# Kernel tuning notes

Hardware: AMD Instinct MI355X
Metric: run time of the kernel (lower is better)

The kernel has to match this reference:

```python
import jax, jax.numpy as jnp
import numpy as np

N, E, D, H, C = 40000, 640000, 128, 4, 32  # nodes, edges, in_hid, heads, out_channels/head
NUM_NODE_TYPE, NUM_EDGE_TYPE = 8, 8
NEG_SLOPE = 0.2
EDGE_TYPE_SELF = 0


def setup_inputs() -> dict:
    key = jax.random.key(0)
    ks = jax.random.split(key, 12)
    x = jax.random.normal(ks[0], (N, D), dtype=jnp.float32)
    # build edges with no self-loops (the module filters src==dst before adding self-loops)
    src = jax.random.randint(ks[1], (E,), 0, N, dtype=jnp.int32)
    off = jax.random.randint(ks[2], (E,), 1, N, dtype=jnp.int32)
    dst = (src + off) % N
    edge_index = jnp.stack([src, dst])  # [2, E]
    node_type = jax.random.randint(ks[3], (N,), 0, NUM_NODE_TYPE, dtype=jnp.int32)
    edge_type = jax.random.randint(ks[4], (E,), 0, NUM_EDGE_TYPE, dtype=jnp.int32)
    g = 0.05
    Wq = jax.random.normal(ks[5], (H * C, D), dtype=jnp.float32) * g
    Wk = jax.random.normal(ks[6], (H * C, D), dtype=jnp.float32) * g
    Wv = jax.random.normal(ks[7], (H * C, D), dtype=jnp.float32) * g
    att_i = jax.random.normal(ks[8], (1, H, C), dtype=jnp.float32) * g
    att_j = jax.random.normal(ks[9], (1, H, C), dtype=jnp.float32) * g
    bias = jnp.zeros((H * C,), dtype=jnp.float32)
    node_emb_table = jax.random.normal(ks[10], (NUM_NODE_TYPE, D), dtype=jnp.float32) * g
    edge_emb_table = jax.random.normal(ks[11], (NUM_EDGE_TYPE, D), dtype=jnp.float32) * g
    return {"x": x, "edge_index": edge_index, "node_type": node_type,
            "edge_type": edge_type, "Wq": Wq, "Wk": Wk, "Wv": Wv,
            "att_i": att_i, "att_j": att_j, "bias": bias,
            "node_emb_table": node_emb_table, "edge_emb_table": edge_emb_table}


def reference(x, edge_index, node_type, edge_type, Wq, Wk, Wv,
              att_i, att_j, bias, node_emb_table, edge_emb_table):
    n = x.shape[0]
    # node-type embedding add
    x = x + node_emb_table[node_type]                       # [N, D]
    xq = x @ Wq.T                                           # [N, H*C]
    # add self-loops (input edges contain no src==dst by construction)
    self_idx = jnp.arange(n, dtype=edge_index.dtype)
    src = jnp.concatenate([edge_index[0], self_idx])        # [E+N]
    dst = jnp.concatenate([edge_index[1], self_idx])        # [E+N]
    et = jnp.concatenate([edge_type,
                          jnp.full((n,), EDGE_TYPE_SELF, dtype=edge_type.dtype)])
    edge_emb = edge_emb_table[et]                           # [E+N, D]
    # message: per-edge gather + K/V linear + additive attention
    x_j = x[src] + edge_emb                                 # [E+N, D]
    xq_i = xq[dst].reshape(-1, H, C)                        # [E+N, H, C]
    x_k = (x_j @ Wk.T).reshape(-1, H, C)
    x_v = (x_j @ Wv.T).reshape(-1, H, C)
    alpha = (xq_i * att_i).sum(-1) + (x_k * att_j).sum(-1)  # [E+N, H]
    alpha = jax.nn.leaky_relu(alpha, NEG_SLOPE)
    # segment softmax over destination nodes (PyG softmax, eps=1e-16)
    amax = jax.ops.segment_max(alpha, dst, num_segments=n)  # [N, H]
    alpha = jnp.exp(alpha - amax[dst])
    denom = jax.ops.segment_sum(alpha, dst, num_segments=n)
    alpha = alpha / (denom[dst] + 1e-16)
    # scatter-add weighted values
    out = jax.ops.segment_sum(x_v * alpha[..., None], dst, num_segments=n)  # [N, H, C]
    return out.reshape(n, H * C) + bias
```

## Files before the change

### kernel.cpp

```cpp
#include <hip/hip_runtime.h>
#include <math.h>

#define NN 40000
#define NE 640000
#define D 128
#define NH 4
#define NC 32
#define NEG 0.2f

#define NBKT 1250
#define NBIN 250
#define SEGC 16

typedef __attribute__((ext_vector_type(8))) short bf16x8;
typedef __attribute__((ext_vector_type(4))) float f32x4;

__device__ __forceinline__ unsigned pack_bf16(float a, float b) {
  unsigned ua = __float_as_uint(a), ub = __float_as_uint(b);
  ua = (ua + 0x7FFFu + ((ua >> 16) & 1u)) >> 16;
  ub = (ub + 0x7FFFu + ((ub >> 16) & 1u)) & 0xFFFF0000u;
  return ub | ua;
}

__device__ __forceinline__ bf16x8 to_bf16x8(float4 a, float4 b) {
  union { bf16x8 v; unsigned u[4]; } r;
  r.u[0] = pack_bf16(a.x, a.y);
  r.u[1] = pack_bf16(a.z, a.w);
  r.u[2] = pack_bf16(b.x, b.y);
  r.u[3] = pack_bf16(b.z, b.w);
  return r.v;
}

__device__ __forceinline__ float4 f4add(float4 a, float4 b) {
  return make_float4(a.x + b.x, a.y + b.y, a.z + b.z, a.w + b.w);
}

__global__ __launch_bounds__(256) void k_pb(
    const int* __restrict__ ei, const int* __restrict__ etype,
    int* __restrict__ bcnt, unsigned* __restrict__ binbuf,
    const float* __restrict__ Wq, const float* __restrict__ Wk,
    const float* __restrict__ Wv,
    const float* __restrict__ att_i, const float* __restrict__ att_j,
    const float* __restrict__ eemb,
    float* __restrict__ ev, float* __restrict__ a_et,
    unsigned* __restrict__ Wvh) {
  __shared__ int shist[1280];
  int b = blockIdx.x, t = threadIdx.x;
  if (b < NBIN) {
    for (int j = t; j < NBKT; j += 256) shist[j] = 0;
    __syncthreads();
    int e0 = b * 2560;
#pragma unroll
    for (int k = 0; k < 10; ++k) {
      int e = e0 + k * 256 + t;
      int src = ei[e];
      int dst = ei[NE + e];
      int et  = etype[e];
      int bk = dst >> 5;
      int r = atomicAdd(&shist[bk], 1);
      if (r < SEGC)
        binbuf[((size_t)bk * NBIN + b) * SEGC + r] =
            (unsigned)src | ((unsigned)et << 16) | ((unsigned)(dst & 31) << 19);
    }
    __syncthreads();
    for (int j = t; j < NBKT; j += 256)
      bcnt[j * NBIN + b] = min(shist[j], SEGC);
    return;
  }
  float* sm = (float*)shist;
  int tb = b - NBIN;
  if (tb == 0) {
    for (int j = t; j < 1024; j += 256) {
      int isq = (j < 512);
      int h = (j >> 7) & 3, d = j & 127;
      const float* __restrict__ Wm = isq ? Wq : Wk;
      const float* __restrict__ am = isq ? att_i : att_j;
      float s = 0.f;
#pragma unroll
      for (int c = 0; c < NC; ++c) s = fmaf(am[h * NC + c], Wm[(h * NC + c) * D + d], s);
      sm[j] = s;
    }
    __syncthreads();
    for (int j = t; j < 1024; j += 256) {
      int r = j >> 6;
      int c2 = (j & 63) * 2;
      float a = 0.f, bb = 0.f;
      if (r < 8) { a = sm[r * 128 + c2]; bb = sm[r * 128 + c2 + 1]; }
      Wvh[(128 + r) * 64 + (j & 63)] = pack_bf16(a, bb);
    }
    if (t < 32) {
      int ty = t >> 2, hh = t & 3;
      const float* wrow = sm + 512 + hh * 128;
      const float* __restrict__ emb = eemb + ty * D;
      float s = 0.f;
#pragma unroll 8
      for (int d = 0; d < D; ++d) s = fmaf(wrow[d], emb[d], s);
      a_et[t] = s;
    }
  } else if (tb <= 8) {
    int ty = tb - 1;
    if (t < 128) sm[t] = eemb[ty * D + t];
    __syncthreads();
    if (t < 128) {
      const float4* __restrict__ wr = (const float4*)(Wv + (size_t)t * D);
      const float4* __restrict__ er = (const float4*)sm;
      float s = 0.f;
#pragma unroll
      for (int k = 0; k < 32; ++k) {
        float4 ww = wr[k], ee = er[k];
        s = fmaf(ww.x, ee.x, s); s = fmaf(ww.y, ee.y, s);
        s = fmaf(ww.z, ee.z, s); s = fmaf(ww.w, ee.w, s);
      }
      ev[ty * D + t] = s;
    }
  } else {
    int j0 = (tb - 9) * 1024;
    for (int j = j0 + t; j < j0 + 1024; j += 256)
      Wvh[j] = pack_bf16(Wv[2 * j], Wv[2 * j + 1]);
  }
}

__global__ __launch_bounds__(256) void k_xv(
    const float* __restrict__ x, const int* __restrict__ node_type,
    const float* __restrict__ nemb, const unsigned* __restrict__ Wvh,
    unsigned* __restrict__ xvh, float* __restrict__ aq, float* __restrict__ ak) {
  int bb = blockIdx.x, t = threadIdx.x;
  int w = t >> 6, l = t & 63;
  int quad = l >> 4, col = l & 15;
  int n0w = bb * 64 + w * 16;
  int node = n0w + col;
  int ntA = node_type[node];
  const float4* __restrict__ xr = (const float4*)(x + (size_t)node * D);
  const float4* __restrict__ nr = (const float4*)(nemb + (size_t)ntA * D);
  bf16x8 afr[4];
#pragma unroll
  for (int s = 0; s < 4; ++s) {
    const float4* p = xr + s * 8 + quad * 2;
    const float4* q4 = nr + s * 8 + quad * 2;
    afr[s] = to_bf16x8(f4add(p[0], q4[0]), f4add(p[1], q4[1]));
  }
  f32x4 acc[9];
#pragma unroll
  for (int ct = 0; ct < 9; ++ct) acc[ct] = (f32x4){0.f, 0.f, 0.f, 0.f};
#pragma unroll
  for (int ct = 0; ct < 9; ++ct) {
    const unsigned* __restrict__ brow = Wvh + (size_t)(ct * 16 + col) * 64;
#pragma unroll
    for (int s = 0; s < 4; ++s) {
      bf16x8 bfr = *(const bf16x8*)(brow + s * 16 + quad * 4);
      acc[ct] = __builtin_amdgcn_mfma_f32_16x16x32_bf16(afr[s], bfr, acc[ct], 0, 0, 0);
    }
  }
  int nodes[4];
#pragma unroll
  for (int r = 0; r < 4; ++r) nodes[r] = n0w + quad * 4 + r;
#pragma unroll
  for (int ct = 0; ct < 8; ++ct) {
#pragma unroll
    for (int r = 0; r < 4; ++r) {
      float val = acc[ct][r];
      float pv = __shfl_xor(val, 1);
      if (!(col & 1)) {
        xvh[nodes[r] * 64 + ct * 8 + (col >> 1)] = pack_bf16(val, pv);
      }
    }
  }
  if (col < 4) {
#pragma unroll
    for (int r = 0; r < 4; ++r) aq[nodes[r] * NH + col] = acc[8][r];
  } else if (col < 8) {
#pragma unroll
    for (int r = 0; r < 4; ++r) ak[nodes[r] * NH + (col - 4)] = acc[8][r];
  }
}

__global__ __launch_bounds__(512) void k_gb(
    const int* __restrict__ bcnt, const unsigned* __restrict__ binbuf,
    const float* __restrict__ aq, const float* __restrict__ ak,
    const float* __restrict__ a_et, const unsigned* __restrict__ xvh,
    const float* __restrict__ ev, const float* __restrict__ bias,
    float* __restrict__ out) {
  __shared__ int lcnt[32];
  __shared__ unsigned csr[2048];
  int b = blockIdx.x, t = threadIdx.x;
  if (t < 32) lcnt[t] = 0;
  __syncthreads();
  if (t < 2 * NBIN) {
    int seg = t >> 1, half = t & 1;
    int cnt = min(bcnt[b * NBIN + seg], SEGC);
    int j0 = half * 8;
    if (cnt > j0) {
      const uint4* __restrict__ sp =
          (const uint4*)(binbuf + ((size_t)b * NBIN + seg) * SEGC) + half * 2;
      uint4 r0 = sp[0], r1 = sp[1];
      unsigned rr[8] = {r0.x, r0.y, r0.z, r0.w, r1.x, r1.y, r1.z, r1.w};
      int j1 = cnt - j0;
#pragma unroll
      for (int j = 0; j < 8; ++j) {
        if (j < j1) {
          unsigned rec = rr[j];
          int loc = (int)(rec >> 19) & 31;
          int r = atomicAdd(&lcnt[loc], 1);
          if (r < 63) csr[(loc << 6) + r] = rec & 0x7FFFFu;
        }
      }
    }
  }
  __syncthreads();
  int w = t >> 6, l = t & 63;
  int g = l >> 3, q = l & 7;
  int h = q >> 1;
  const uint4* __restrict__ xv4 = (const uint4*)xvh;
  const float4* __restrict__ ep = (const float4*)(ev + g * D + 16 * q);
  float4 ea0 = ep[0], ea1 = ep[1], ea2 = ep[2], ea3 = ep[3];
#pragma unroll 1
  for (int j4 = 0; j4 < 4; ++j4) {
    int loc = (w << 2) + j4;
    int n = (b << 5) + loc;
    float aqh = aq[n * NH + h];
    int deg = min(lcnt[loc], 63);
    int m = deg + 1;
    float acc[16];
#pragma unroll
    for (int k = 0; k < 16; ++k) acc[k] = 0.f;
    float ps[8];
#pragma unroll
    for (int k = 0; k < 8; ++k) ps[k] = 0.f;
    int iters = (m + 7) >> 3;
    int i = g;
    bool val = (i < m);
    unsigned rec = (val && i < deg) ? csr[(loc << 6) + i] : (unsigned)n;
    int src = (int)(rec & 0xFFFFu), etc = (int)(rec >> 16);
    float sA = ak[src * NH + h] + a_et[etc * NH + h];
    uint4 vb0 = xv4[src * 16 + 2 * q];
    uint4 vb1 = xv4[src * 16 + 2 * q + 1];
    for (int it = 0; it < iters; ++it) {
      int i2 = i + 8;
      bool v2 = (i2 < m);
      float sAn = 0.f; int etn = 0;
      uint4 vb0n = make_uint4(0, 0, 0, 0), vb1n = make_uint4(0, 0, 0, 0);
      if (it + 1 < iters) {
        unsigned rec2 = (v2 && i2 < deg) ? csr[(loc << 6) + i2] : (unsigned)n;
        int s2 = (int)(rec2 & 0xFFFFu);
        etn = (int)(rec2 >> 16);
        sAn = ak[s2 * NH + h] + a_et[etn * NH + h];
        vb0n = xv4[s2 * 16 + 2 * q];
        vb1n = xv4[s2 * 16 + 2 * q + 1];
      }
      float s = aqh + sA;
      s = (s > 0.f) ? s : NEG * s;
      float p = val ? __expf(s) : 0.f;
#pragma unroll
      for (int tt = 0; tt < 8; ++tt) ps[tt] += (etc == tt) ? p : 0.f;
      float f[16];
      f[0]  = __uint_as_float(vb0.x << 16); f[1]  = __uint_as_float(vb0.x & 0xFFFF0000u);
      f[2]  = __uint_as_float(vb0.y << 16); f[3]  = __uint_as_float(vb0.y & 0xFFFF0000u);
      f[4]  = __uint_as_float(vb0.z << 16); f[5]  = __uint_as_float(vb0.z & 0xFFFF0000u);
      f[6]  = __uint_as_float(vb0.w << 16); f[7]  = __uint_as_float(vb0.w & 0xFFFF0000u);
      f[8]  = __uint_as_float(vb1.x << 16); f[9]  = __uint_as_float(vb1.x & 0xFFFF0000u);
      f[10] = __uint_as_float(vb1.y << 16); f[11] = __uint_as_float(vb1.y & 0xFFFF0000u);
      f[12] = __uint_as_float(vb1.z << 16); f[13] = __uint_as_float(vb1.z & 0xFFFF0000u);
      f[14] = __uint_as_float(vb1.w << 16); f[15] = __uint_as_float(vb1.w & 0xFFFF0000u);
#pragma unroll
      for (int k = 0; k < 16; ++k) acc[k] = fmaf(p, f[k], acc[k]);
      i = i2; val = v2; sA = sAn; etc = etn; vb0 = vb0n; vb1 = vb1n;
    }
#pragma unroll
    for (int tt = 0; tt < 8; ++tt) {
      ps[tt] += __shfl_xor(ps[tt], 8);
      ps[tt] += __shfl_xor(ps[tt], 16);
      ps[tt] += __shfl_xor(ps[tt], 32);
    }
    float dsum = ((ps[0] + ps[1]) + (ps[2] + ps[3])) + ((ps[4] + ps[5]) + (ps[6] + ps[7]));
    float psg = ps[0];
#pragma unroll
    for (int tt = 1; tt < 8; ++tt) psg = (g == tt) ? ps[tt] : psg;
    acc[0]  = fmaf(psg, ea0.x, acc[0]);
    acc[1]  = fmaf(psg, ea0.y, acc[1]);
    acc[2]  = fmaf(psg, ea0.z, acc[2]);
    acc[3]  = fmaf(psg, ea0.w, acc[3]);
    acc[4]  = fmaf(psg, ea1.x, acc[4]);
    acc[5]  = fmaf(psg, ea1.y, acc[5]);
    acc[6]  = fmaf(psg, ea1.z, acc[6]);
    acc[7]  = fmaf(psg, ea1.w, acc[7]);
    acc[8]  = fmaf(psg, ea2.x, acc[8]);
    acc[9]  = fmaf(psg, ea2.y, acc[9]);
    acc[10] = fmaf(psg, ea2.z, acc[10]);
    acc[11] = fmaf(psg, ea2.w, acc[11]);
    acc[12] = fmaf(psg, ea3.x, acc[12]);
    acc[13] = fmaf(psg, ea3.y, acc[13]);
    acc[14] = fmaf(psg, ea3.z, acc[14]);
    acc[15] = fmaf(psg, ea3.w, acc[15]);
#pragma unroll
    for (int k = 0; k < 16; ++k) {
      acc[k] += __shfl_xor(acc[k], 8);
      acc[k] += __shfl_xor(acc[k], 16);
      acc[k] += __shfl_xor(acc[k], 32);
    }
    if (g == 0) {
      float inv = 1.f / (dsum + 1e-16f);
      const float4* __restrict__ b4 = (const float4*)(bias + 16 * q);
      float4* __restrict__ op = (float4*)(out + (size_t)n * D + 16 * q);
#pragma unroll
      for (int k4 = 0; k4 < 4; ++k4) {
        float4 bb = b4[k4];
        op[k4] = make_float4(acc[4 * k4 + 0] * inv + bb.x,
                             acc[4 * k4 + 1] * inv + bb.y,
                             acc[4 * k4 + 2] * inv + bb.z,
                             acc[4 * k4 + 3] * inv + bb.w);
      }
    }
  }
}

extern "C" void kernel_launch(void* const* d_in, const int* in_sizes, int n_in,
                              void* d_out, int out_size, void* d_ws, size_t ws_size,
                              hipStream_t stream) {
  const float* x      = (const float*)d_in[0];
  const int*   ei     = (const int*)d_in[1];
  const int*   ntype  = (const int*)d_in[2];
  const int*   etype  = (const int*)d_in[3];
  const float* Wq     = (const float*)d_in[4];
  const float* Wk     = (const float*)d_in[5];
  const float* Wv     = (const float*)d_in[6];
  const float* att_i  = (const float*)d_in[7];
  const float* att_j  = (const float*)d_in[8];
  const float* bias   = (const float*)d_in[9];
  const float* nemb   = (const float*)d_in[10];
  const float* eemb   = (const float*)d_in[11];
  float* out = (float*)d_out;

  float* ws     = (float*)d_ws;
  unsigned* xvh = (unsigned*)ws;
  float* aq     = ws + (size_t)NN * 64;
  float* ak     = aq + NN * NH;
  float* ev     = ak + NN * NH;
  float* a_et   = ev + 1024;
  unsigned* Wvh = (unsigned*)(a_et + 32);
  int* bcnt     = (int*)(Wvh + 9216);
  unsigned* binbuf = (unsigned*)(bcnt + 312512);

  k_pb<<<dim3(NBIN + 17), dim3(256), 0, stream>>>(ei, etype, bcnt, binbuf,
                                                  Wq, Wk, Wv, att_i, att_j, eemb,
                                                  ev, a_et, Wvh);
  k_xv<<<dim3(625), dim3(256), 0, stream>>>(x, ntype, nemb, Wvh, xvh, aq, ak);
  k_gb<<<dim3(NBKT), dim3(512), 0, stream>>>(bcnt, binbuf, aq, ak, a_et,
                                             xvh, ev, bias, out);
}
```

Baseline: 169.2 us.

## Pack bin counts into records, stage bins in LDS, and use 64-node buckets

The edge binning now stages each block's per-bucket records in shared memory. It stores the record count in the top bits of the first record, then writes whole 64-byte segments to global memory with vector stores, so the separate count array goes away. Buckets double to 64 destination nodes and each bin covers half as many edges. The gather kernel reads each segment with four 16-byte loads and processes 64 nodes per block. This removes the count reads and the scattered partial stores, but it always writes and reads full segments, including empty slots, which adds memory traffic.

```diff
diff --git a/kernel.cpp b/kernel.cpp
--- a/kernel.cpp
+++ b/kernel.cpp
@@ -8,8 +8,8 @@
 #define NC 32
 #define NEG 0.2f
 
-#define NBKT 1250
-#define NBIN 250
+#define NBKT 625
+#define NBIN 500
 #define SEGC 16
 
 typedef __attribute__((ext_vector_type(8))) short bf16x8;
@@ -37,37 +37,50 @@
 
 __global__ __launch_bounds__(256) void k_pb(
     const int* __restrict__ ei, const int* __restrict__ etype,
-    int* __restrict__ bcnt, unsigned* __restrict__ binbuf,
+    unsigned* __restrict__ binbuf,
     const float* __restrict__ Wq, const float* __restrict__ Wk,
     const float* __restrict__ Wv,
     const float* __restrict__ att_i, const float* __restrict__ att_j,
     const float* __restrict__ eemb,
     float* __restrict__ ev, float* __restrict__ a_et,
     unsigned* __restrict__ Wvh) {
-  __shared__ int shist[1280];
+  __shared__ unsigned smem[10640];
   int b = blockIdx.x, t = threadIdx.x;
+
   if (b < NBIN) {
-    for (int j = t; j < NBKT; j += 256) shist[j] = 0;
-    __syncthreads();
-    int e0 = b * 2560;
-#pragma unroll
-    for (int k = 0; k < 10; ++k) {
+    unsigned* lbuf = smem;
+    int* hist = (int*)(smem + 10000);
+    for (int j = t; j < NBKT; j += 256) hist[j] = 0;
+    __syncthreads();
+    int e0 = b * 1280;
+#pragma unroll
+    for (int k = 0; k < 5; ++k) {
       int e = e0 + k * 256 + t;
       int src = ei[e];
       int dst = ei[NE + e];
       int et  = etype[e];
-      int bk = dst >> 5;
-      int r = atomicAdd(&shist[bk], 1);
+      int bk = dst >> 6;
+      int r = atomicAdd(&hist[bk], 1);
       if (r < SEGC)
-        binbuf[((size_t)bk * NBIN + b) * SEGC + r] =
-            (unsigned)src | ((unsigned)et << 16) | ((unsigned)(dst & 31) << 19);
-    }
-    __syncthreads();
-    for (int j = t; j < NBKT; j += 256)
-      bcnt[j * NBIN + b] = min(shist[j], SEGC);
+        lbuf[bk * SEGC + r] =
+            (unsigned)src | ((unsigned)et << 16) | ((unsigned)(dst & 63) << 19);
+    }
+    __syncthreads();
+    for (int j = t; j < NBKT; j += 256) {
+      unsigned c = (unsigned)min(hist[j], SEGC);
+      unsigned s0 = (c == 0) ? 0u : (lbuf[j * SEGC] & 0x01FFFFFFu);
+      lbuf[j * SEGC] = s0 | (c << 27);
+    }
+    __syncthreads();
+    for (int j = t; j < NBKT; j += 256) {
+      const uint4* __restrict__ s4 = (const uint4*)(lbuf + j * SEGC);
+      uint4* __restrict__ d4 = (uint4*)(binbuf + ((size_t)j * NBIN + b) * SEGC);
+      d4[0] = s4[0]; d4[1] = s4[1]; d4[2] = s4[2]; d4[3] = s4[3];
+    }
     return;
   }
-  float* sm = (float*)shist;
+
+  float* sm = (float*)smem;
   int tb = b - NBIN;
   if (tb == 0) {
     for (int j = t; j < 1024; j += 256) {
@@ -175,34 +188,33 @@
 }
 
 __global__ __launch_bounds__(512) void k_gb(
-    const int* __restrict__ bcnt, const unsigned* __restrict__ binbuf,
+    const unsigned* __restrict__ binbuf,
     const float* __restrict__ aq, const float* __restrict__ ak,
     const float* __restrict__ a_et, const unsigned* __restrict__ xvh,
     const float* __restrict__ ev, const float* __restrict__ bias,
     float* __restrict__ out) {
-  __shared__ int lcnt[32];
-  __shared__ unsigned csr[2048];
+  __shared__ int lcnt[64];
+  __shared__ unsigned csr[4096];
   int b = blockIdx.x, t = threadIdx.x;
-  if (t < 32) lcnt[t] = 0;
+  if (t < 64) lcnt[t] = 0;
   __syncthreads();
-  if (t < 2 * NBIN) {
-    int seg = t >> 1, half = t & 1;
-    int cnt = min(bcnt[b * NBIN + seg], SEGC);
-    int j0 = half * 8;
-    if (cnt > j0) {
-      const uint4* __restrict__ sp =
-          (const uint4*)(binbuf + ((size_t)b * NBIN + seg) * SEGC) + half * 2;
-      uint4 r0 = sp[0], r1 = sp[1];
-      unsigned rr[8] = {r0.x, r0.y, r0.z, r0.w, r1.x, r1.y, r1.z, r1.w};
-      int j1 = cnt - j0;
-#pragma unroll
-      for (int j = 0; j < 8; ++j) {
-        if (j < j1) {
-          unsigned rec = rr[j];
-          int loc = (int)(rec >> 19) & 31;
-          int r = atomicAdd(&lcnt[loc], 1);
-          if (r < 63) csr[(loc << 6) + r] = rec & 0x7FFFFu;
-        }
+  if (t < NBIN) {
+    const unsigned* __restrict__ sp = binbuf + ((size_t)b * NBIN + t) * SEGC;
+    uint4 a0 = *(const uint4*)sp;
+    uint4 a1 = *(const uint4*)(sp + 4);
+    uint4 a2 = *(const uint4*)(sp + 8);
+    uint4 a3 = *(const uint4*)(sp + 12);
+    unsigned rr[16] = {a0.x, a0.y, a0.z, a0.w, a1.x, a1.y, a1.z, a1.w,
+                       a2.x, a2.y, a2.z, a2.w, a3.x, a3.y, a3.z, a3.w};
+    int cnt = (int)(rr[0] >> 27);
+    rr[0] &= 0x01FFFFFFu;
+#pragma unroll
+    for (int j = 0; j < SEGC; ++j) {
+      if (j < cnt) {
+        unsigned rec = rr[j];
+        int loc = (int)(rec >> 19) & 63;
+        int r = atomicAdd(&lcnt[loc], 1);
+        if (r < 63) csr[(loc << 6) + r] = rec & 0x7FFFFu;
       }
     }
   }
@@ -214,9 +226,9 @@
   const float4* __restrict__ ep = (const float4*)(ev + g * D + 16 * q);
   float4 ea0 = ep[0], ea1 = ep[1], ea2 = ep[2], ea3 = ep[3];
 #pragma unroll 1
-  for (int j4 = 0; j4 < 4; ++j4) {
-    int loc = (w << 2) + j4;
-    int n = (b << 5) + loc;
+  for (int j4 = 0; j4 < 8; ++j4) {
+    int loc = (w << 3) + j4;
+    int n = (b << 6) + loc;
     float aqh = aq[n * NH + h];
     int deg = min(lcnt[loc], 63);
     int m = deg + 1;
@@ -337,13 +349,12 @@
   float* ev     = ak + NN * NH;
   float* a_et   = ev + 1024;
   unsigned* Wvh = (unsigned*)(a_et + 32);
-  int* bcnt     = (int*)(Wvh + 9216);
-  unsigned* binbuf = (unsigned*)(bcnt + 312512);
-
-  k_pb<<<dim3(NBIN + 17), dim3(256), 0, stream>>>(ei, etype, bcnt, binbuf,
+  unsigned* binbuf = (unsigned*)(Wvh + 9216);
+
+  k_pb<<<dim3(NBIN + 17), dim3(256), 0, stream>>>(ei, etype, binbuf,
                                                   Wq, Wk, Wv, att_i, att_j, eemb,
                                                   ev, a_et, Wvh);
   k_xv<<<dim3(625), dim3(256), 0, stream>>>(x, ntype, nemb, Wvh, xvh, aq, ak);
-  k_gb<<<dim3(NBKT), dim3(512), 0, stream>>>(bcnt, binbuf, aq, ak, a_et,
+  k_gb<<<dim3(NBKT), dim3(512), 0, stream>>>(binbuf, aq, ak, a_et,
                                              xvh, ev, bias, out);
 }
```

Result: slower. 176.8 us (+4.5%).

## Stage bucketed edge records in LDS and embed counts in record headers

Applied to the files above, without the earlier changes.

The binning kernel now builds each block's bucket segments in shared memory over two passes of 625 buckets, then writes them out as full 64-byte vector stores instead of scattered 4-byte global writes. The per-segment count is packed into the top bits of the first record, which removes the separate count array and its extra read in the gather kernel. This trades scattered writes for coalesced ones, but every segment is now written in full, including empty ones. It also adds a second pass over the edge inputs and uses about 42KB of LDS per block, which may lower occupancy.

```diff
diff --git a/kernel.cpp b/kernel.cpp
--- a/kernel.cpp
+++ b/kernel.cpp
@@ -37,37 +37,58 @@
 
 __global__ __launch_bounds__(256) void k_pb(
     const int* __restrict__ ei, const int* __restrict__ etype,
-    int* __restrict__ bcnt, unsigned* __restrict__ binbuf,
+    unsigned* __restrict__ binbuf,
     const float* __restrict__ Wq, const float* __restrict__ Wk,
     const float* __restrict__ Wv,
     const float* __restrict__ att_i, const float* __restrict__ att_j,
     const float* __restrict__ eemb,
     float* __restrict__ ev, float* __restrict__ a_et,
     unsigned* __restrict__ Wvh) {
-  __shared__ int shist[1280];
+  __shared__ unsigned smem[10640];
   int b = blockIdx.x, t = threadIdx.x;
+
   if (b < NBIN) {
-    for (int j = t; j < NBKT; j += 256) shist[j] = 0;
-    __syncthreads();
+    unsigned* lbuf = smem;
+    int* hist = (int*)(smem + 10000);
     int e0 = b * 2560;
-#pragma unroll
-    for (int k = 0; k < 10; ++k) {
-      int e = e0 + k * 256 + t;
-      int src = ei[e];
-      int dst = ei[NE + e];
-      int et  = etype[e];
-      int bk = dst >> 5;
-      int r = atomicAdd(&shist[bk], 1);
-      if (r < SEGC)
-        binbuf[((size_t)bk * NBIN + b) * SEGC + r] =
-            (unsigned)src | ((unsigned)et << 16) | ((unsigned)(dst & 31) << 19);
-    }
-    __syncthreads();
-    for (int j = t; j < NBKT; j += 256)
-      bcnt[j * NBIN + b] = min(shist[j], SEGC);
+#pragma unroll 1
+    for (int pass = 0; pass < 2; ++pass) {
+      int bk0 = pass * 625;
+      for (int j = t; j < 625; j += 256) hist[j] = 0;
+      __syncthreads();
+#pragma unroll
+      for (int k = 0; k < 10; ++k) {
+        int e = e0 + k * 256 + t;
+        int src = ei[e];
+        int dst = ei[NE + e];
+        int et  = etype[e];
+        int bk = (dst >> 5) - bk0;
+        if (bk >= 0 && bk < 625) {
+          int r = atomicAdd(&hist[bk], 1);
+          if (r < SEGC)
+            lbuf[bk * SEGC + r] =
+                (unsigned)src | ((unsigned)et << 16) | ((unsigned)(dst & 31) << 19);
+        }
+      }
+      __syncthreads();
+      for (int j = t; j < 625; j += 256) {
+        unsigned c = (unsigned)min(hist[j], SEGC);
+        unsigned s0 = (c == 0) ? 0u : (lbuf[j * SEGC] & 0x01FFFFFFu);
+        lbuf[j * SEGC] = s0 | (c << 27);
+      }
+      __syncthreads();
+      for (int j = t; j < 625; j += 256) {
+        const uint4* __restrict__ s4 = (const uint4*)(lbuf + j * SEGC);
+        uint4* __restrict__ d4 =
+            (uint4*)(binbuf + ((size_t)(bk0 + j) * NBIN + b) * SEGC);
+        d4[0] = s4[0]; d4[1] = s4[1]; d4[2] = s4[2]; d4[3] = s4[3];
+      }
+      __syncthreads();
+    }
     return;
   }
-  float* sm = (float*)shist;
+
+  float* sm = (float*)smem;
   int tb = b - NBIN;
   if (tb == 0) {
     for (int j = t; j < 1024; j += 256) {
@@ -175,7 +196,7 @@
 }
 
 __global__ __launch_bounds__(512) void k_gb(
-    const int* __restrict__ bcnt, const unsigned* __restrict__ binbuf,
+    const unsigned* __restrict__ binbuf,
     const float* __restrict__ aq, const float* __restrict__ ak,
     const float* __restrict__ a_et, const unsigned* __restrict__ xvh,
     const float* __restrict__ ev, const float* __restrict__ bias,
@@ -187,17 +208,18 @@
   __syncthreads();
   if (t < 2 * NBIN) {
     int seg = t >> 1, half = t & 1;
-    int cnt = min(bcnt[b * NBIN + seg], SEGC);
-    int j0 = half * 8;
-    if (cnt > j0) {
-      const uint4* __restrict__ sp =
-          (const uint4*)(binbuf + ((size_t)b * NBIN + seg) * SEGC) + half * 2;
-      uint4 r0 = sp[0], r1 = sp[1];
-      unsigned rr[8] = {r0.x, r0.y, r0.z, r0.w, r1.x, r1.y, r1.z, r1.w};
-      int j1 = cnt - j0;
+    const unsigned* __restrict__ sp = binbuf + ((size_t)b * NBIN + seg) * SEGC;
+    int cnt = (int)(sp[0] >> 27);
+    int base = half * 8;
+    if (cnt > base) {
+      uint4 a0 = *(const uint4*)(sp + base);
+      uint4 a1 = *(const uint4*)(sp + base + 4);
+      unsigned rr[8] = {a0.x, a0.y, a0.z, a0.w, a1.x, a1.y, a1.z, a1.w};
+      if (half == 0) rr[0] &= 0x01FFFFFFu;
+      int jn = min(cnt - base, 8);
 #pragma unroll
       for (int j = 0; j < 8; ++j) {
-        if (j < j1) {
+        if (j < jn) {
           unsigned rec = rr[j];
           int loc = (int)(rec >> 19) & 31;
           int r = atomicAdd(&lcnt[loc], 1);
@@ -337,13 +359,12 @@
   float* ev     = ak + NN * NH;
   float* a_et   = ev + 1024;
   unsigned* Wvh = (unsigned*)(a_et + 32);
-  int* bcnt     = (int*)(Wvh + 9216);
-  unsigned* binbuf = (unsigned*)(bcnt + 312512);
-
-  k_pb<<<dim3(NBIN + 17), dim3(256), 0, stream>>>(ei, etype, bcnt, binbuf,
+  unsigned* binbuf = (unsigned*)(Wvh + 9216);
+
+  k_pb<<<dim3(NBIN + 17), dim3(256), 0, stream>>>(ei, etype, binbuf,
                                                   Wq, Wk, Wv, att_i, att_j, eemb,
                                                   ev, a_et, Wvh);
   k_xv<<<dim3(625), dim3(256), 0, stream>>>(x, ntype, nemb, Wvh, xvh, aq, ak);
-  k_gb<<<dim3(NBKT), dim3(512), 0, stream>>>(bcnt, binbuf, aq, ak, a_et,
+  k_gb<<<dim3(NBKT), dim3(512), 0, stream>>>(binbuf, aq, ak, a_et,
                                              xvh, ev, bias, out);
 }
```

New measurement: 169.2 us. No clear change (+0.0%).
